# Optimization experiments

Hardware: AMD Instinct MI355X
Metric: run time of the kernel (lower is better)

## Reference

```python
import jax, jax.numpy as jnp
import numpy as np

N_NODES = 50000
N_EDGES = 800000
IN_DIM, HIDDEN, Z_DIM = 32, 64, 32


def gcn_conv(x, W, b, src, dst, n):
    """PyG-style GCNConv: h = D^{-1/2}(A+I)D^{-1/2} (x W) + b."""
    h = x @ W  # [N, out]
    loop = jnp.arange(n, dtype=src.dtype)
    s = jnp.concatenate([src, loop])  # add self-loops
    d = jnp.concatenate([dst, loop])
    deg = jax.ops.segment_sum(jnp.ones(s.shape, h.dtype), d, num_segments=n)
    dinv = jax.lax.rsqrt(jnp.maximum(deg, jnp.asarray(1.0, h.dtype)))
    norm = dinv[s] * dinv[d]                       # [E+N]
    msg = h[s] * norm[:, None]                     # gather + scale
    out = jax.ops.segment_sum(msg, d, num_segments=n)  # scatter-add
    return out + b


def setup_inputs() -> dict:
    key = jax.random.key(0)
    ks = jax.random.split(key, 8)
    sc = lambda fan_in: 1.0 / np.sqrt(fan_in)
    x = jax.random.normal(ks[0], (N_NODES, IN_DIM), jnp.float32)
    edge_index = jax.random.randint(ks[1], (2, N_EDGES), 0, N_NODES, jnp.int64)
    W1 = jax.random.normal(ks[2], (IN_DIM, HIDDEN), jnp.float32) * sc(IN_DIM)
    b1 = jnp.zeros((HIDDEN,), jnp.float32)
    W2 = jax.random.normal(ks[3], (HIDDEN, HIDDEN), jnp.float32) * sc(HIDDEN)
    b2 = jnp.zeros((HIDDEN,), jnp.float32)
    W_mu = jax.random.normal(ks[4], (HIDDEN, Z_DIM), jnp.float32) * sc(HIDDEN)
    b_mu = jnp.zeros((Z_DIM,), jnp.float32)
    W_lv = jax.random.normal(ks[5], (HIDDEN, Z_DIM), jnp.float32) * sc(HIDDEN)
    b_lv = jnp.zeros((Z_DIM,), jnp.float32)
    eps = jax.random.normal(ks[6], (N_NODES, Z_DIM), jnp.float32)
    return {"x": x, "edge_index": edge_index, "W1": W1, "b1": b1, "W2": W2,
            "b2": b2, "W_mu": W_mu, "b_mu": b_mu, "W_lv": W_lv, "b_lv": b_lv,
            "eps": eps}


def reference(x, edge_index, W1, b1, W2, b2, W_mu, b_mu, W_lv, b_lv, eps):
    src, dst = edge_index[0], edge_index[1]
    n = x.shape[0]
    h = jax.nn.relu(gcn_conv(x, W1, b1, src, dst, n))
    h = jax.nn.relu(gcn_conv(h, W2, b2, src, dst, n))
    # dropout p=0.0 -> identity
    mu = gcn_conv(h, W_mu, b_mu, src, dst, n)
    logvar = gcn_conv(h, W_lv, b_lv, src, dst, n)
    z = mu + jnp.exp(0.5 * logvar) * eps  # reparametrize
    return (z, mu, logvar)
```

## Files before the change

### kernel.cpp

```cpp
#include <hip/hip_runtime.h>
#include <math.h>

#define N_NODES 50000
#define N_EDGES 800000
#define IN_DIM 32
#define HIDDEN 64
#define Z_DIM 32
#define SCAN_B 256
#define NB_SCAN ((N_NODES + SCAN_B - 1) / SCAN_B)
#define N_XCD 8
#define NPX ((N_NODES + N_XCD - 1) / N_XCD)
#define SLICE 2048
#define N_SLICE ((N_EDGES + SLICE - 1) / SLICE)
#define SCAT_B (N_SLICE * N_XCD)
#define FB 2048
#define CPAD 16

__device__ __forceinline__ unsigned short f2bf(float f) {
    unsigned int u = __float_as_uint(f);
    u += 0x7fffu + ((u >> 16) & 1u);
    return (unsigned short)(u >> 16);
}

__device__ __forceinline__ int detect64(const int* raw) {
    int lane = threadIdx.x & 63;
    int odd = raw[2 * lane + 1];
    unsigned long long b = __ballot(odd != 0);
    return (b == 0ULL) ? 1 : 0;
}

__device__ __forceinline__ void fma8(float w, uint4 f, float acc[8]) {
    acc[0] = fmaf(w, __uint_as_float(f.x << 16),         acc[0]);
    acc[1] = fmaf(w, __uint_as_float(f.x & 0xffff0000u), acc[1]);
    acc[2] = fmaf(w, __uint_as_float(f.y << 16),         acc[2]);
    acc[3] = fmaf(w, __uint_as_float(f.y & 0xffff0000u), acc[3]);
    acc[4] = fmaf(w, __uint_as_float(f.z << 16),         acc[4]);
    acc[5] = fmaf(w, __uint_as_float(f.z & 0xffff0000u), acc[5]);
    acc[6] = fmaf(w, __uint_as_float(f.w << 16),         acc[6]);
    acc[7] = fmaf(w, __uint_as_float(f.w & 0xffff0000u), acc[7]);
}
__device__ __forceinline__ void mul8(float w, uint4 f, float acc[8]) {
    acc[0] = w * __uint_as_float(f.x << 16);
    acc[1] = w * __uint_as_float(f.x & 0xffff0000u);
    acc[2] = w * __uint_as_float(f.y << 16);
    acc[3] = w * __uint_as_float(f.y & 0xffff0000u);
    acc[4] = w * __uint_as_float(f.z << 16);
    acc[5] = w * __uint_as_float(f.z & 0xffff0000u);
    acc[6] = w * __uint_as_float(f.w << 16);
    acc[7] = w * __uint_as_float(f.w & 0xffff0000u);
}

__global__ void prep_a_kernel(const float* __restrict__ x, unsigned short* __restrict__ xb,
                              const void* __restrict__ raw, ushort2* __restrict__ ep0,
                              int* __restrict__ cnt) {
    int is64 = detect64((const int*)raw);
    int i = blockIdx.x * 256 + threadIdx.x;
    if (i < N_NODES * IN_DIM) xb[i] = f2bf(x[i]);
    if (i < N_NODES * CPAD) cnt[i] = 0;
    if (i < N_EDGES) {
        int s, d;
        if (is64) {
            s = (int)((const long long*)raw)[i];
            d = (int)((const long long*)raw)[N_EDGES + i];
        } else {
            s = ((const int*)raw)[i];
            d = ((const int*)raw)[N_EDGES + i];
        }
        ep0[i] = make_ushort2((unsigned short)s, (unsigned short)d);
    }
}

__global__ __launch_bounds__(256) void hist_kernel(const ushort2* __restrict__ ep0,
                                                   int* __restrict__ cnt,
                                                   unsigned short* __restrict__ rank) {
    int xcd = blockIdx.x % N_XCD;
    int sl  = blockIdx.x / N_XCD;
    int lo  = xcd * NPX, hi = lo + NPX;
    int base = sl * SLICE;
#pragma unroll
    for (int j = 0; j < SLICE / 256; j++) {
        int e = base + j * 256 + threadIdx.x;
        if (e < N_EDGES) {
            int d = ep0[e].y;
            if (d >= lo && d < hi)
                rank[e] = (unsigned short)atomicAdd(&cnt[(size_t)d * CPAD], 1);
        }
    }
}

__global__ void scan1_kernel(const int* __restrict__ cnt, int* __restrict__ pre,
                             int* __restrict__ bsum, float* __restrict__ dinv) {
    __shared__ int s[SCAN_B];
    int t = threadIdx.x;
    int g = blockIdx.x * SCAN_B + t;
    int v = (g < N_NODES) ? cnt[(size_t)g * CPAD] : 0;
    if (g < N_NODES) dinv[g] = rsqrtf((float)(v + 1));
    s[t] = v;
    __syncthreads();
    for (int o = 1; o < SCAN_B; o <<= 1) {
        int add = (t >= o) ? s[t - o] : 0;
        __syncthreads();
        s[t] += add;
        __syncthreads();
    }
    if (g < N_NODES) pre[g] = s[t] - v;
    if (t == SCAN_B - 1) bsum[blockIdx.x] = s[t];
}

#define BSUM_SCAN_PROLOGUE(bsum, sb, sx)                                    \
    {                                                                       \
        int t_ = threadIdx.x;                                               \
        int bv_ = (t_ < NB_SCAN) ? bsum[t_] : 0;                            \
        sb[t_] = bv_;                                                       \
        __syncthreads();                                                    \
        for (int o_ = 1; o_ < 256; o_ <<= 1) {                              \
            int a_ = (t_ >= o_) ? sb[t_ - o_] : 0;                          \
            __syncthreads();                                                \
            sb[t_] += a_;                                                   \
            __syncthreads();                                                \
        }                                                                   \
        sx[t_] = sb[t_] - bv_;                                              \
        __syncthreads();                                                    \
    }

__global__ __launch_bounds__(256) void scatter_kernel(
        const ushort2* __restrict__ ep0, const unsigned short* __restrict__ rank,
        const int* __restrict__ pre, const int* __restrict__ bsum,
        const float* __restrict__ dinv, int2* __restrict__ ep) {
    __shared__ int sb[256];
    __shared__ int sx[256];
    BSUM_SCAN_PROLOGUE(bsum, sb, sx)
    int base = blockIdx.x * SLICE;
#pragma unroll
    for (int j = 0; j < SLICE / 256; j++) {
        int e = base + j * 256 + threadIdx.x;
        if (e < N_EDGES) {
            ushort2 sd = ep0[e];
            int d = sd.y;
            int p = pre[d] + sx[d >> 8] + (int)rank[e];
            int s = sd.x;
            ep[p] = make_int2(s, __float_as_int(dinv[s]));
        }
    }
}

__device__ __forceinline__ void agg64(int e0, int e1, int2 pr,
                                      const int2* __restrict__ ep,
                                      const uint4* __restrict__ g4,
                                      int2* eb, int lane, int gsel, int c,
                                      float acc[8]) {
    for (int b0 = e0; b0 < e1; b0 += 64) {
        int cnt = e1 - b0; cnt = cnt > 64 ? 64 : cnt;
        eb[lane] = pr;
        for (int j = 0; j < cnt; j += 16) {
            int2 ew0 = eb[j + gsel];
            int2 ew1 = eb[j + 8 + gsel];
            uint4 f0 = g4[(size_t)ew0.x * 8 + c];
            uint4 f1 = g4[(size_t)ew1.x * 8 + c];
            fma8(__int_as_float(ew0.y), f0, acc);
            fma8(__int_as_float(ew1.y), f1, acc);
        }
        if (b0 + 64 < e1) {
            pr = make_int2(0, 0);
            int idx = b0 + 64 + lane;
            if (idx < e1) pr = ep[idx];
        }
    }
}

__device__ __forceinline__ void agg32(int e0, int e1, int2 pr,
                                      const int2* __restrict__ ep,
                                      const uint4* __restrict__ x4,
                                      int2* eb, int lane, int gsel, int c,
                                      float acc[8]) {
    for (int b0 = e0; b0 < e1; b0 += 64) {
        int cnt = e1 - b0; cnt = cnt > 64 ? 64 : cnt;
        eb[lane] = pr;
        for (int j = 0; j < cnt; j += 32) {
            int2 ew0 = eb[j + gsel];
            int2 ew1 = eb[j + 16 + gsel];
            uint4 f0 = x4[(size_t)ew0.x * 4 + c];
            uint4 f1 = x4[(size_t)ew1.x * 4 + c];
            fma8(__int_as_float(ew0.y), f0, acc);
            fma8(__int_as_float(ew1.y), f1, acc);
        }
        if (b0 + 64 < e1) {
            pr = make_int2(0, 0);
            int idx = b0 + 64 + lane;
            if (idx < e1) pr = ep[idx];
        }
    }
}

__global__ __launch_bounds__(256, 4) void fused_layer32_kernel(
        const int* __restrict__ pre, const int* __restrict__ bsum,
        const int2* __restrict__ ep, const float* __restrict__ dinv,
        const unsigned short* __restrict__ xb,
        const float* __restrict__ W1, const float* __restrict__ b1,
        unsigned short* __restrict__ out) {
    __shared__ int sb[256];
    __shared__ int sx[256];
    __shared__ int2 ebuf[4][64];
    __shared__ float sq[4][32];
    BSUM_SCAN_PROLOGUE(bsum, sb, sx)
    int lane = threadIdx.x & 63;
    int wav  = threadIdx.x >> 6;
    int gsel = lane >> 2;
    int c    = lane & 3;
    const uint4* x4 = (const uint4*)xb;
    int2* eb = &ebuf[wav][0];
    float wcol[IN_DIM];
#pragma unroll
    for (int k = 0; k < IN_DIM; k++) wcol[k] = W1[k * 64 + lane];
    float bb = b1[lane];
    int wid = __builtin_amdgcn_readfirstlane((int)((blockIdx.x * blockDim.x + threadIdx.x) >> 6));
    int nw  = (gridDim.x * blockDim.x) >> 6;
    int v = wid;
    if (v >= N_NODES) return;
    int e0 = pre[v] + sx[v >> 8];
    int e1 = (v + 1 < N_NODES) ? pre[v + 1] + sx[(v + 1) >> 8] : N_EDGES;
    float dv = dinv[v];
    uint4 hv = x4[(size_t)v * 4 + c];
    int2 pr = make_int2(0, 0);
    if (lane < e1 - e0) pr = ep[e0 + lane];
    while (v < N_NODES) {
        int vn = v + nw;
        int e0n = 0, e1n = 0;
        float dvn = 0.0f;
        uint4 hvn = make_uint4(0, 0, 0, 0);
        int2 prn = make_int2(0, 0);
        if (vn < N_NODES) {
            e0n = pre[vn] + sx[vn >> 8];
            e1n = (vn + 1 < N_NODES) ? pre[vn + 1] + sx[(vn + 1) >> 8] : N_EDGES;
            dvn = dinv[vn];
            hvn = x4[(size_t)vn * 4 + c];
            if (lane < e1n - e0n) prn = ep[e0n + lane];
        }
        float sv = (gsel == 0) ? dv : 0.0f;
        float acc[8];
        mul8(sv, hv, acc);
        agg32(e0, e1, pr, ep, x4, eb, lane, gsel, c, acc);
#pragma unroll
        for (int i = 0; i < 8; i++) {
            acc[i] += __shfl_xor(acc[i], 4);
            acc[i] += __shfl_xor(acc[i], 8);
            acc[i] += __shfl_xor(acc[i], 16);
            acc[i] += __shfl_xor(acc[i], 32);
        }
        if (lane < 4) {
            float4* qd = (float4*)(&sq[wav][lane * 8]);
            qd[0] = make_float4(dv * acc[0], dv * acc[1], dv * acc[2], dv * acc[3]);
            qd[1] = make_float4(dv * acc[4], dv * acc[5], dv * acc[6], dv * acc[7]);
        }
        float o = bb;
        const float4* q4 = (const float4*)(&sq[wav][0]);
#pragma unroll
        for (int k = 0; k < IN_DIM / 4; k++) {
            float4 tq = q4[k];
            o = fmaf(tq.x, wcol[4 * k + 0], o);
            o = fmaf(tq.y, wcol[4 * k + 1], o);
            o = fmaf(tq.z, wcol[4 * k + 2], o);
            o = fmaf(tq.w, wcol[4 * k + 3], o);
        }
        out[(size_t)v * 64 + lane] = f2bf(fmaxf(o, 0.0f));
        v = vn; e0 = e0n; e1 = e1n; dv = dvn; hv = hvn; pr = prn;
    }
}

__global__ __launch_bounds__(256, 4) void fused_layer64_kernel(
        const int* __restrict__ pre, const int* __restrict__ bsum,
        const int2* __restrict__ ep, const float* __restrict__ dinv,
        const unsigned short* __restrict__ g,
        const float* __restrict__ W, const float* __restrict__ bias,
        unsigned short* __restrict__ out) {
    __shared__ int sb[256];
    __shared__ int sx[256];
    __shared__ int2 ebuf[4][64];
    __shared__ float sq[4][64];
    BSUM_SCAN_PROLOGUE(bsum, sb, sx)
    int lane = threadIdx.x & 63;
    int wav  = threadIdx.x >> 6;
    int gsel = lane >> 3;
    int c    = lane & 7;
    const uint4* g4 = (const uint4*)g;
    int2* eb = &ebuf[wav][0];
    float wcol[HIDDEN];
#pragma unroll
    for (int k = 0; k < HIDDEN; k++) wcol[k] = W[k * 64 + lane];
    float bb = bias[lane];
    int wid = __builtin_amdgcn_readfirstlane((int)((blockIdx.x * blockDim.x + threadIdx.x) >> 6));
    int nw  = (gridDim.x * blockDim.x) >> 6;
    int v = wid;
    if (v >= N_NODES) return;
    int e0 = pre[v] + sx[v >> 8];
    int e1 = (v + 1 < N_NODES) ? pre[v + 1] + sx[(v + 1) >> 8] : N_EDGES;
    float dv = dinv[v];
    uint4 hv = g4[(size_t)v * 8 + c];
    int2 pr = make_int2(0, 0);
    if (lane < e1 - e0) pr = ep[e0 + lane];
    while (v < N_NODES) {
        int vn = v + nw;
        int e0n = 0, e1n = 0;
        float dvn = 0.0f;
        uint4 hvn = make_uint4(0, 0, 0, 0);
        int2 prn = make_int2(0, 0);
        if (vn < N_NODES) {
            e0n = pre[vn] + sx[vn >> 8];
            e1n = (vn + 1 < N_NODES) ? pre[vn + 1] + sx[(vn + 1) >> 8] : N_EDGES;
            dvn = dinv[vn];
            hvn = g4[(size_t)vn * 8 + c];
            if (lane < e1n - e0n) prn = ep[e0n + lane];
        }
        float sv = (gsel == 0) ? dv : 0.0f;
        float acc[8];
        mul8(sv, hv, acc);
        agg64(e0, e1, pr, ep, g4, eb, lane, gsel, c, acc);
#pragma unroll
        for (int i = 0; i < 8; i++) {
            acc[i] += __shfl_xor(acc[i], 8);
            acc[i] += __shfl_xor(acc[i], 16);
            acc[i] += __shfl_xor(acc[i], 32);
        }
        if (lane < 8) {
            float4* qd = (float4*)(&sq[wav][lane * 8]);
            qd[0] = make_float4(dv * acc[0], dv * acc[1], dv * acc[2], dv * acc[3]);
            qd[1] = make_float4(dv * acc[4], dv * acc[5], dv * acc[6], dv * acc[7]);
        }
        float o = bb;
        const float4* q4 = (const float4*)(&sq[wav][0]);
#pragma unroll
        for (int k = 0; k < HIDDEN / 4; k++) {
            float4 tq = q4[k];
            o = fmaf(tq.x, wcol[4 * k + 0], o);
            o = fmaf(tq.y, wcol[4 * k + 1], o);
            o = fmaf(tq.z, wcol[4 * k + 2], o);
            o = fmaf(tq.w, wcol[4 * k + 3], o);
        }
        out[(size_t)v * 64 + lane] = f2bf(fmaxf(o, 0.0f));
        v = vn; e0 = e0n; e1 = e1n; dv = dvn; hv = hvn; pr = prn;
    }
}

__global__ __launch_bounds__(256, 4) void fused_head_kernel(
        const int* __restrict__ pre, const int* __restrict__ bsum,
        const int2* __restrict__ ep, const float* __restrict__ dinv,
        const unsigned short* __restrict__ g,
        const float* __restrict__ Wmu, const float* __restrict__ Wlv,
        const float* __restrict__ bmu, const float* __restrict__ blv,
        const float* __restrict__ eps, float* __restrict__ outz) {
    __shared__ int sb[256];
    __shared__ int sx[256];
    __shared__ int2 ebuf[4][64];
    __shared__ float sq[4][64];
    BSUM_SCAN_PROLOGUE(bsum, sb, sx)
    int lane = threadIdx.x & 63;
    int wav  = threadIdx.x >> 6;
    int gsel = lane >> 3;
    int c    = lane & 7;
    int f = lane & 31;
    bool hi = lane >= 32;
    const uint4* g4 = (const uint4*)g;
    int2* eb = &ebuf[wav][0];
    float wcol[HIDDEN];
#pragma unroll
    for (int k = 0; k < HIDDEN; k++)
        wcol[k] = hi ? Wlv[k * 32 + f] : Wmu[k * 32 + f];
    float bb = hi ? blv[f] : bmu[f];
    float* z  = outz;
    float* mu = outz + (size_t)N_NODES * Z_DIM;
    float* lv = outz + 2 * (size_t)N_NODES * Z_DIM;
    int wid = __builtin_amdgcn_readfirstlane((int)((blockIdx.x * blockDim.x + threadIdx.x) >> 6));
    int nw  = (gridDim.x * blockDim.x) >> 6;
    int v = wid;
    if (v >= N_NODES) return;
    int e0 = pre[v] + sx[v >> 8];
    int e1 = (v + 1 < N_NODES) ? pre[v + 1] + sx[(v + 1) >> 8] : N_EDGES;
    float dv = dinv[v];
    uint4 hv = g4[(size_t)v * 8 + c];
    int2 pr = make_int2(0, 0);
    if (lane < e1 - e0) pr = ep[e0 + lane];
    while (v < N_NODES) {
        int vn = v + nw;
        int e0n = 0, e1n = 0;
        float dvn = 0.0f;
        uint4 hvn = make_uint4(0, 0, 0, 0);
        int2 prn = make_int2(0, 0);
        if (vn < N_NODES) {
            e0n = pre[vn] + sx[vn >> 8];
            e1n = (vn + 1 < N_NODES) ? pre[vn + 1] + sx[(vn + 1) >> 8] : N_EDGES;
            dvn = dinv[vn];
            hvn = g4[(size_t)vn * 8 + c];
            if (lane < e1n - e0n) prn = ep[e0n + lane];
        }
        float sv = (gsel == 0) ? dv : 0.0f;
        float acc[8];
        mul8(sv, hv, acc);
        agg64(e0, e1, pr, ep, g4, eb, lane, gsel, c, acc);
#pragma unroll
        for (int i = 0; i < 8; i++) {
            acc[i] += __shfl_xor(acc[i], 8);
            acc[i] += __shfl_xor(acc[i], 16);
            acc[i] += __shfl_xor(acc[i], 32);
        }
        if (lane < 8) {
            float4* qd = (float4*)(&sq[wav][lane * 8]);
            qd[0] = make_float4(dv * acc[0], dv * acc[1], dv * acc[2], dv * acc[3]);
            qd[1] = make_float4(dv * acc[4], dv * acc[5], dv * acc[6], dv * acc[7]);
        }
        float m = bb;
        const float4* q4 = (const float4*)(&sq[wav][0]);
#pragma unroll
        for (int k = 0; k < HIDDEN / 4; k++) {
            float4 tq = q4[k];
            m = fmaf(tq.x, wcol[4 * k + 0], m);
            m = fmaf(tq.y, wcol[4 * k + 1], m);
            m = fmaf(tq.z, wcol[4 * k + 2], m);
            m = fmaf(tq.w, wcol[4 * k + 3], m);
        }
        float ev = eps[(size_t)v * Z_DIM + f];
        float t  = expf(0.5f * m) * ev;
        float tlo = __shfl(t, lane | 32);
        size_t o = (size_t)v * Z_DIM + f;
        if (!hi) { mu[o] = m; z[o] = m + tlo; }
        else     { lv[o] = m; }
        v = vn; e0 = e0n; e1 = e1n; dv = dvn; hv = hvn; pr = prn;
    }
}

extern "C" void kernel_launch(void* const* d_in, const int* in_sizes, int n_in,
                              void* d_out, int out_size, void* d_ws, size_t ws_size,
                              hipStream_t stream) {
    const float* x   = (const float*)d_in[0];
    const void*  ei  = d_in[1];
    const float* W1  = (const float*)d_in[2];
    const float* b1  = (const float*)d_in[3];
    const float* W2  = (const float*)d_in[4];
    const float* b2  = (const float*)d_in[5];
    const float* Wmu = (const float*)d_in[6];
    const float* bmu = (const float*)d_in[7];
    const float* Wlv = (const float*)d_in[8];
    const float* blv = (const float*)d_in[9];
    const float* eps = (const float*)d_in[10];
    float* out = (float*)d_out;
    (void)in_sizes; (void)n_in; (void)out_size; (void)ws_size;

    char* ws = (char*)d_ws;
    size_t off = 0;
    auto alloc = [&](size_t bytes) -> void* {
        void* p = ws + off;
        off += (bytes + 255) & ~(size_t)255;
        return p;
    };
    int2*           ep     = (int2*)alloc(sizeof(int2) * N_EDGES);
    ushort2*        ep0    = (ushort2*)alloc(sizeof(ushort2) * N_EDGES);
    unsigned short* rank   = (unsigned short*)alloc(sizeof(short) * N_EDGES);
    int*            pre    = (int*)alloc(sizeof(int) * (N_NODES + 1));
    int*            cnt    = (int*)alloc(sizeof(int) * (size_t)N_NODES * CPAD);
    float*          dinv   = (float*)alloc(sizeof(float) * N_NODES);
    int*            bsum   = (int*)alloc(sizeof(int) * 256);
    unsigned short* xb     = (unsigned short*)alloc(sizeof(short) * (size_t)N_NODES * IN_DIM);
    unsigned short* G      = (unsigned short*)alloc(sizeof(short) * (size_t)N_NODES * HIDDEN);
    unsigned short* H      = (unsigned short*)alloc(sizeof(short) * (size_t)N_NODES * HIDDEN);

    prep_a_kernel<<<(N_NODES * IN_DIM + 255) / 256, 256, 0, stream>>>(x, xb, ei, ep0, cnt);
    hist_kernel<<<SCAT_B, 256, 0, stream>>>(ep0, cnt, rank);
    scan1_kernel<<<NB_SCAN, SCAN_B, 0, stream>>>(cnt, pre, bsum, dinv);
    scatter_kernel<<<N_SLICE, 256, 0, stream>>>(ep0, rank, pre, bsum, dinv, ep);
    fused_layer32_kernel<<<FB, 256, 0, stream>>>(pre, bsum, ep, dinv, xb, W1, b1, H);
    fused_layer64_kernel<<<FB, 256, 0, stream>>>(pre, bsum, ep, dinv, H, W2, b2, G);
    fused_head_kernel<<<FB, 256, 0, stream>>>(pre, bsum, ep, dinv, G, Wmu, Wlv, bmu, blv, eps, out);
}
```

Measured before the change: 250.9 us.

## Split dense-projection FMA chains, relax launch bounds, and halve FB block constant

The per-node dense projection in all three fused kernels now uses four independent accumulators instead of one serial FMA chain, which shortens the dependency latency. The min-blocks-per-SM hint is dropped from __launch_bounds__, so the compiler may use more registers at the cost of possible lower occupancy. FB is halved, which changes the work or grid granularity of whatever uses it. The reassociated sum changes floating-point rounding slightly.

```diff
diff --git a/kernel.cpp b/kernel.cpp
--- a/kernel.cpp
+++ b/kernel.cpp
@@ -13,7 +13,7 @@
 #define SLICE 2048
 #define N_SLICE ((N_EDGES + SLICE - 1) / SLICE)
 #define SCAT_B (N_SLICE * N_XCD)
-#define FB 2048
+#define FB 1024
 #define CPAD 16
 
 __device__ __forceinline__ unsigned short f2bf(float f) {
@@ -192,7 +192,7 @@
     }
 }
 
-__global__ __launch_bounds__(256, 4) void fused_layer32_kernel(
+__global__ __launch_bounds__(256) void fused_layer32_kernel(
         const int* __restrict__ pre, const int* __restrict__ bsum,
         const int2* __restrict__ ep, const float* __restrict__ dinv,
         const unsigned short* __restrict__ xb,
@@ -252,22 +252,23 @@
             qd[0] = make_float4(dv * acc[0], dv * acc[1], dv * acc[2], dv * acc[3]);
             qd[1] = make_float4(dv * acc[4], dv * acc[5], dv * acc[6], dv * acc[7]);
         }
-        float o = bb;
+        float o0 = bb, o1 = 0.0f, o2 = 0.0f, o3 = 0.0f;
         const float4* q4 = (const float4*)(&sq[wav][0]);
 #pragma unroll
         for (int k = 0; k < IN_DIM / 4; k++) {
             float4 tq = q4[k];
-            o = fmaf(tq.x, wcol[4 * k + 0], o);
-            o = fmaf(tq.y, wcol[4 * k + 1], o);
-            o = fmaf(tq.z, wcol[4 * k + 2], o);
-            o = fmaf(tq.w, wcol[4 * k + 3], o);
-        }
+            o0 = fmaf(tq.x, wcol[4 * k + 0], o0);
+            o1 = fmaf(tq.y, wcol[4 * k + 1], o1);
+            o2 = fmaf(tq.z, wcol[4 * k + 2], o2);
+            o3 = fmaf(tq.w, wcol[4 * k + 3], o3);
+        }
+        float o = (o0 + o1) + (o2 + o3);
         out[(size_t)v * 64 + lane] = f2bf(fmaxf(o, 0.0f));
         v = vn; e0 = e0n; e1 = e1n; dv = dvn; hv = hvn; pr = prn;
     }
 }
 
-__global__ __launch_bounds__(256, 4) void fused_layer64_kernel(
+__global__ __launch_bounds__(256) void fused_layer64_kernel(
         const int* __restrict__ pre, const int* __restrict__ bsum,
         const int2* __restrict__ ep, const float* __restrict__ dinv,
         const unsigned short* __restrict__ g,
@@ -326,22 +327,23 @@
             qd[0] = make_float4(dv * acc[0], dv * acc[1], dv * acc[2], dv * acc[3]);
             qd[1] = make_float4(dv * acc[4], dv * acc[5], dv * acc[6], dv * acc[7]);
         }
-        float o = bb;
+        float o0 = bb, o1 = 0.0f, o2 = 0.0f, o3 = 0.0f;
         const float4* q4 = (const float4*)(&sq[wav][0]);
 #pragma unroll
         for (int k = 0; k < HIDDEN / 4; k++) {
             float4 tq = q4[k];
-            o = fmaf(tq.x, wcol[4 * k + 0], o);
-            o = fmaf(tq.y, wcol[4 * k + 1], o);
-            o = fmaf(tq.z, wcol[4 * k + 2], o);
-            o = fmaf(tq.w, wcol[4 * k + 3], o);
-        }
+            o0 = fmaf(tq.x, wcol[4 * k + 0], o0);
+            o1 = fmaf(tq.y, wcol[4 * k + 1], o1);
+            o2 = fmaf(tq.z, wcol[4 * k + 2], o2);
+            o3 = fmaf(tq.w, wcol[4 * k + 3], o3);
+        }
+        float o = (o0 + o1) + (o2 + o3);
         out[(size_t)v * 64 + lane] = f2bf(fmaxf(o, 0.0f));
         v = vn; e0 = e0n; e1 = e1n; dv = dvn; hv = hvn; pr = prn;
     }
 }
 
-__global__ __launch_bounds__(256, 4) void fused_head_kernel(
+__global__ __launch_bounds__(256) void fused_head_kernel(
         const int* __restrict__ pre, const int* __restrict__ bsum,
         const int2* __restrict__ ep, const float* __restrict__ dinv,
         const unsigned short* __restrict__ g,
@@ -407,16 +409,17 @@
             qd[0] = make_float4(dv * acc[0], dv * acc[1], dv * acc[2], dv * acc[3]);
             qd[1] = make_float4(dv * acc[4], dv * acc[5], dv * acc[6], dv * acc[7]);
         }
-        float m = bb;
+        float m0 = bb, m1 = 0.0f, m2 = 0.0f, m3 = 0.0f;
         const float4* q4 = (const float4*)(&sq[wav][0]);
 #pragma unroll
         for (int k = 0; k < HIDDEN / 4; k++) {
             float4 tq = q4[k];
-            m = fmaf(tq.x, wcol[4 * k + 0], m);
-            m = fmaf(tq.y, wcol[4 * k + 1], m);
-            m = fmaf(tq.z, wcol[4 * k + 2], m);
-            m = fmaf(tq.w, wcol[4 * k + 3], m);
-        }
+            m0 = fmaf(tq.x, wcol[4 * k + 0], m0);
+            m1 = fmaf(tq.y, wcol[4 * k + 1], m1);
+            m2 = fmaf(tq.z, wcol[4 * k + 2], m2);
+            m3 = fmaf(tq.w, wcol[4 * k + 3], m3);
+        }
+        float m = (m0 + m1) + (m2 + m3);
         float ev = eps[(size_t)v * Z_DIM + f];
         float t  = expf(0.5f * m) * ev;
         float tlo = __shfl(t, lane | 32);
```

Measured after the change: 249.1 us. Within noise of the previous version (-0.7%).
